# Kernel tuning notes

Hardware: AMD Instinct MI355X
Metric: run time of the kernel (lower is better)

## Reference

```python
import jax, jax.numpy as jnp
import numpy as np

EMB = 128
HEADS = 4
HEAD_DIM = 128  # concat=False: out_channels per head = embedding_dim
LAYERS = 4
BOARD_WIDTH = 8
FC1 = 64
NEG_SLOPE = 0.2  # GATv2 LeakyReLU default
N_CELLS = 200_000
N_PIECES = 100_000
N_EDGES = 500_000
N_GRAPHS = 256


def setup_inputs() -> dict:
    key = jax.random.key(0)
    ks = jax.random.split(key, 24)
    cell_x = jnp.zeros((N_CELLS,), jnp.int32)  # cell vocab size is 1
    piece_x = jax.random.randint(ks[0], (N_PIECES, 1), 0, 2, dtype=jnp.int32)
    edge_src = jax.random.randint(ks[1], (N_EDGES,), 0, N_PIECES, dtype=jnp.int32)
    edge_dst = jax.random.randint(ks[2], (N_EDGES,), 0, N_CELLS, dtype=jnp.int32)
    cell_batch = jnp.sort(jax.random.randint(ks[3], (N_CELLS,), 0, N_GRAPHS, dtype=jnp.int32))

    HD = HEADS * HEAD_DIM
    s_emb = 1.0
    s_lin = 1.0 / np.sqrt(EMB)
    cell_emb = jax.random.normal(ks[4], (1, EMB), jnp.float32) * s_emb
    piece_emb = jax.random.normal(ks[5], (2, EMB), jnp.float32) * s_emb
    W_l = jax.random.normal(ks[6], (LAYERS, EMB, HD), jnp.float32) * s_lin
    b_l = jnp.zeros((LAYERS, HD), jnp.float32)
    W_r = jax.random.normal(ks[7], (LAYERS, EMB, HD), jnp.float32) * s_lin
    b_r = jnp.zeros((LAYERS, HD), jnp.float32)
    att = jax.random.normal(ks[8], (LAYERS, HEADS, HEAD_DIM), jnp.float32) * (1.0 / np.sqrt(HEAD_DIM))
    conv_bias = jnp.zeros((LAYERS, EMB), jnp.float32)
    fc1_w = jax.random.normal(ks[9], (EMB, FC1), jnp.float32) * s_lin
    fc1_b = jnp.zeros((FC1,), jnp.float32)
    policy_w = jax.random.normal(ks[10], (FC1, BOARD_WIDTH), jnp.float32) * (1.0 / np.sqrt(FC1))
    policy_b = jnp.zeros((BOARD_WIDTH,), jnp.float32)
    value_w = jax.random.normal(ks[11], (FC1, 1), jnp.float32) * (1.0 / np.sqrt(FC1))
    value_b = jnp.zeros((1,), jnp.float32)
    return {
        "cell_x": cell_x, "piece_x": piece_x, "edge_src": edge_src,
        "edge_dst": edge_dst, "cell_batch": cell_batch,
        "cell_emb": cell_emb, "piece_emb": piece_emb,
        "W_l": W_l, "b_l": b_l, "W_r": W_r, "b_r": b_r,
        "att": att, "conv_bias": conv_bias,
        "fc1_w": fc1_w, "fc1_b": fc1_b,
        "policy_w": policy_w, "policy_b": policy_b,
        "value_w": value_w, "value_b": value_b,
    }


def _gatv2_layer(piece, cell, edge_src, edge_dst, Wl, bl, Wr, br, a, bias):
    P, C = piece.shape[0], cell.shape[0]
    x_src = (piece @ Wl + bl).reshape(P, HEADS, HEAD_DIM)
    x_dst = (cell @ Wr + br).reshape(C, HEADS, HEAD_DIM)
    xs = x_src[edge_src]                       # [E,H,D] gather
    e = jax.nn.leaky_relu(xs + x_dst[edge_dst], NEG_SLOPE)
    logits = jnp.einsum('ehd,hd->eh', e, a)    # [E,H]
    # segment softmax over edges sharing the same destination cell
    m = jax.ops.segment_max(logits, edge_dst, num_segments=C)
    ex = jnp.exp(logits - m[edge_dst])
    denom = jax.ops.segment_sum(ex, edge_dst, num_segments=C)
    alpha = ex / denom[edge_dst]               # [E,H]
    msg = xs * alpha[:, :, None]               # [E,H,D]
    out = jax.ops.segment_sum(msg, edge_dst, num_segments=C)  # [C,H,D]
    return out.mean(axis=1) + bias             # concat=False -> mean over heads


def reference(cell_x, piece_x, edge_src, edge_dst, cell_batch,
              cell_emb, piece_emb, W_l, b_l, W_r, b_r, att, conv_bias,
              fc1_w, fc1_b, policy_w, policy_b, value_w, value_b):
    cell = cell_emb[cell_x]                    # [C,128]
    piece = piece_emb[piece_x.squeeze(-1)]     # [P,128], never updated (HeteroConv only emits dst type)
    for l in range(LAYERS):
        cell = _gatv2_layer(piece, cell, edge_src, edge_dst,
                            W_l[l], b_l[l], W_r[l], b_r[l], att[l], conv_bias[l])
        cell = jax.nn.relu(cell)               # dropout: eval-mode identity
    # global mean pool over cells per graph
    sums = jax.ops.segment_sum(cell, cell_batch, num_segments=N_GRAPHS)
    cnts = jax.ops.segment_sum(jnp.ones((cell.shape[0],), cell.dtype), cell_batch, num_segments=N_GRAPHS)
    graph_emb = sums / jnp.maximum(cnts, 1.0)[:, None]
    h = jax.nn.relu(graph_emb @ fc1_w + fc1_b)
    policy_logits = h @ policy_w + policy_b
    value = jnp.tanh(h @ value_w + value_b)
    return (policy_logits, value)
```

## Files before the change

kernel.cpp:

```cpp
#include <hip/hip_runtime.h>
#include <math.h>

#define NC 200000
#define NE 500000
#define NP 100000
#define NG 256
#define NLAYERS 4
#define NKEY 256
#define CLAMP 15
#define NSLOPE 0.2f
#define R 8

#define O_CNT 0u
#define O_TB  6400000u
#define O_XS  6412800u
#define O_GB  6429184u
#define O_TAB 6430336u

#define ZB   1563
#define TBB  13
#define XSB  16
#define GBB  782
#define PREP_BLOCKS (ZB + TBB + XSB + GBB)

__device__ __forceinline__ float lrelu(float x) { return x > 0.f ? x : NSLOPE * x; }

__global__ void k_prep(int4* __restrict__ zbase,
                       const int* __restrict__ piece_x,
                       unsigned* __restrict__ tb,
                       const float* __restrict__ piece_emb,
                       const float* __restrict__ W_l,
                       const float* __restrict__ b_l,
                       float* __restrict__ xs,
                       const int* __restrict__ cell_batch,
                       int* __restrict__ gb) {
  int b = blockIdx.x, tid = threadIdx.x;
  if (b < ZB) {
    int i4 = b * 256 + tid;
    if (i4 < (R * NC) / 4) zbase[i4] = make_int4(0, 0, 0, 0);
  } else if (b < ZB + TBB) {
    int j = (b - ZB) * 256 + tid;
    if (j < NP / 32) {
      unsigned w = 0;
      const int* p = piece_x + j * 32;
      #pragma unroll
      for (int k = 0; k < 32; ++k) w |= (unsigned)(p[k] & 1) << k;
      tb[j] = w;
    }
  } else if (b < ZB + TBB + XSB) {
    int idx = (b - ZB - TBB) * 256 + tid;
    int l = idx >> 10, t = (idx >> 9) & 1, j = idx & 511;
    float acc = b_l[l * 512 + j];
    const float* pe = piece_emb + t * 128;
    const float* W = W_l + l * 65536;
    #pragma unroll 8
    for (int d = 0; d < 128; ++d) acc = fmaf(pe[d], W[d * 512 + j], acc);
    xs[idx] = acc;
  } else {
    int i = (b - ZB - TBB - XSB) * 256 + tid;
    if (i < NC) {
      int bi = cell_batch[i];
      int bn = (i + 1 < NC) ? cell_batch[i + 1] : NG;
      if (i == 0) for (int g = 0; g <= bi; ++g) gb[g] = 0;
      for (int g = bi + 1; g <= bn; ++g) gb[g] = i + 1;
    }
  }
}

__global__ void __launch_bounds__(256)
k_count(const unsigned* __restrict__ tb,
        const int* __restrict__ esrc,
        const int* __restrict__ edst,
        int* __restrict__ cnt) {
  unsigned xcc;
  asm volatile("s_getreg_b32 %0, hwreg(HW_REG_XCC_ID)" : "=s"(xcc));
  int* base = cnt + (xcc & (R - 1)) * NC;
  int gid = blockIdx.x * blockDim.x + threadIdx.x;
  if (gid >= NE / 4) return;
  int4 s4 = *(const int4*)(esrc + gid * 4);
  int4 d4 = *(const int4*)(edst + gid * 4);
  int t0 = (tb[s4.x >> 5] >> (s4.x & 31)) & 1;
  int t1 = (tb[s4.y >> 5] >> (s4.y & 31)) & 1;
  int t2 = (tb[s4.z >> 5] >> (s4.z & 31)) & 1;
  int t3 = (tb[s4.w >> 5] >> (s4.w & 31)) & 1;
  atomicAdd(&base[d4.x], 1 << (t0 << 4));
  atomicAdd(&base[d4.y], 1 << (t1 << 4));
  atomicAdd(&base[d4.z], 1 << (t2 << 4));
  atomicAdd(&base[d4.w], 1 << (t3 << 4));
}

__global__ void __launch_bounds__(512)
k_layers4(const float* __restrict__ cell_emb,
          const float* __restrict__ W_r, const float* __restrict__ b_r,
          const float* __restrict__ xs,  const float* __restrict__ att,
          const float* __restrict__ conv_bias,
          float* __restrict__ tab) {
  __shared__ float cell[128];
  __shared__ float part[8][2];
  __shared__ float wgt[8];
  int tid = threadIdx.x;
  int key = blockIdx.x;
  int n0 = key >> 4, n1 = key & 15;
  if (tid < 128) cell[tid] = cell_emb[tid];
  __syncthreads();

  for (int l = 0; l < NLAYERS; ++l) {
    const float* Wl  = W_r + (size_t)l * 65536;
    const float* xsL = xs + l * 1024;
    float acc = b_r[l * 512 + tid];
    #pragma unroll 16
    for (int d = 0; d < 128; ++d)
      acc = fmaf(cell[d], Wl[d * 512 + tid], acc);
    float av = att[l * 512 + tid];
    float p0 = lrelu(xsL[tid] + acc) * av;
    float p1 = lrelu(xsL[512 + tid] + acc) * av;
    #pragma unroll
    for (int m = 32; m >= 1; m >>= 1) {
      p0 += __shfl_xor(p0, m);
      p1 += __shfl_xor(p1, m);
    }
    int w = tid >> 6, lane = tid & 63;
    if (lane == 0) { part[w][0] = p0; part[w][1] = p1; }
    __syncthreads();
    if (tid < 4) {
      float L0 = part[2 * tid][0] + part[2 * tid + 1][0];
      float L1 = part[2 * tid][1] + part[2 * tid + 1][1];
      float ww0 = 0.f, ww1 = 0.f;
      if (n0 + n1 > 0) {
        float m = -1e30f;
        if (n0 > 0) m = L0;
        if (n1 > 0) m = fmaxf(m, L1);
        float e0 = (n0 > 0) ? (float)n0 * expf(L0 - m) : 0.f;
        float e1 = (n1 > 0) ? (float)n1 * expf(L1 - m) : 0.f;
        float inv = 1.f / (e0 + e1);
        ww0 = e0 * inv; ww1 = e1 * inv;
      }
      wgt[tid] = ww0; wgt[4 + tid] = ww1;
    }
    __syncthreads();
    if (tid < 128) {
      float o = conv_bias[l * 128 + tid];
      #pragma unroll
      for (int h = 0; h < 4; ++h)
        o += 0.25f * (wgt[h]     * xsL[h * 128 + tid] +
                      wgt[4 + h] * xsL[512 + h * 128 + tid]);
      o = fmaxf(o, 0.f);
      cell[tid] = o;
      if (l == NLAYERS - 1) tab[key * 128 + tid] = o;
    }
    __syncthreads();
  }
}

__global__ void __launch_bounds__(256)
k_poolhead(const int* __restrict__ gb, const unsigned* __restrict__ cnt,
           const float* __restrict__ tab,
           const float* __restrict__ fc1_w, const float* __restrict__ fc1_b,
           const float* __restrict__ pol_w, const float* __restrict__ pol_b,
           const float* __restrict__ val_w, const float* __restrict__ val_b,
           float* __restrict__ out) {
  __shared__ int hist[NKEY];
  __shared__ int klist[NKEY];
  __shared__ int wcnt[4];
  __shared__ float emb[128];
  __shared__ float hbuf[64];
  int g = blockIdx.x, tid = threadIdx.x;
  hist[tid] = 0;
  __syncthreads();
  int lo = gb[g], hi = gb[g + 1];
  for (int c = lo + tid; c < hi; c += 256) {
    unsigned v = 0;
    #pragma unroll
    for (int r = 0; r < R; ++r) v += cnt[c + r * NC];
    int n0 = min((int)(v & 0xffffu), CLAMP);
    int n1 = min((int)(v >> 16), CLAMP);
    atomicAdd(&hist[(n0 << 4) | n1], 1);
  }
  __syncthreads();
  unsigned long long m = __ballot(hist[tid] != 0);
  int w = tid >> 6, lane = tid & 63;
  if (lane == 0) wcnt[w] = __popcll(m);
  __syncthreads();
  int basep = 0;
  #pragma unroll
  for (int i = 0; i < 4; ++i) if (i < w) basep += wcnt[i];
  if (hist[tid] != 0)
    klist[basep + __popcll(m & ((1ull << lane) - 1ull))] = tid;
  __syncthreads();
  int kn = wcnt[0] + wcnt[1] + wcnt[2] + wcnt[3];
  if (tid < 128) {
    float acc = 0.f;
    for (int i = 0; i < kn; ++i) {
      int k = klist[i];
      acc = fmaf((float)hist[k], tab[k * 128 + tid], acc);
    }
    emb[tid] = acc / fmaxf((float)(hi - lo), 1.f);
  }
  __syncthreads();
  if (tid < 64) {
    float a = fc1_b[tid];
    #pragma unroll 8
    for (int d = 0; d < 128; ++d) a = fmaf(emb[d], fc1_w[d * 64 + tid], a);
    hbuf[tid] = fmaxf(a, 0.f);
  }
  __syncthreads();
  if (tid < 8) {
    float p = pol_b[tid];
    #pragma unroll
    for (int k = 0; k < 64; ++k) p = fmaf(hbuf[k], pol_w[k * 8 + tid], p);
    out[g * 8 + tid] = p;
  } else if (tid == 8) {
    float v = val_b[0];
    #pragma unroll
    for (int k = 0; k < 64; ++k) v = fmaf(hbuf[k], val_w[k], v);
    out[NG * 8 + g] = tanhf(v);
  }
}

extern "C" void kernel_launch(void* const* d_in, const int* in_sizes, int n_in,
                              void* d_out, int out_size, void* d_ws, size_t ws_size,
                              hipStream_t stream) {
  (void)in_sizes; (void)n_in; (void)out_size; (void)ws_size;
  const int*   piece_x   = (const int*)d_in[1];
  const int*   edge_src  = (const int*)d_in[2];
  const int*   edge_dst  = (const int*)d_in[3];
  const int*   cell_batch= (const int*)d_in[4];
  const float* cell_emb  = (const float*)d_in[5];
  const float* piece_emb = (const float*)d_in[6];
  const float* W_l       = (const float*)d_in[7];
  const float* b_l       = (const float*)d_in[8];
  const float* W_r       = (const float*)d_in[9];
  const float* b_r       = (const float*)d_in[10];
  const float* att       = (const float*)d_in[11];
  const float* conv_bias = (const float*)d_in[12];
  const float* fc1_w     = (const float*)d_in[13];
  const float* fc1_b     = (const float*)d_in[14];
  const float* pol_w     = (const float*)d_in[15];
  const float* pol_b     = (const float*)d_in[16];
  const float* val_w     = (const float*)d_in[17];
  const float* val_b     = (const float*)d_in[18];
  float* out = (float*)d_out;

  char* ws = (char*)d_ws;
  int*      cnt  = (int*)(ws + O_CNT);
  unsigned* cntu = (unsigned*)(ws + O_CNT);
  unsigned* tb   = (unsigned*)(ws + O_TB);
  float*    xs   = (float*)(ws + O_XS);
  int*      gb   = (int*)(ws + O_GB);
  float*    tab  = (float*)(ws + O_TAB);

  k_prep<<<PREP_BLOCKS, 256, 0, stream>>>((int4*)ws, piece_x, tb, piece_emb,
                                          W_l, b_l, xs, cell_batch, gb);
  k_count<<<(NE / 4 + 255) / 256, 256, 0, stream>>>(tb, edge_src, edge_dst, cnt);
  k_layers4<<<NKEY, 512, 0, stream>>>(cell_emb, W_r, b_r, xs, att, conv_bias, tab);
  k_poolhead<<<NG, 256, 0, stream>>>(gb, cntu, tab,
                                     fc1_w, fc1_b, pol_w, pol_b,
                                     val_w, val_b, out);
}
```

Before: 59.52 us.

## Fuse all stages into one cooperative persistent kernel with grid syncs

Replaces the four separate launches with a single cooperative kernel of 256 blocks × 512 threads that runs the prep, edge-count, layer-table and pool/head phases, separated by grid-wide barriers. The edge counting is merged into the layer phase, so its atomics can overlap with the per-key layer computation, which does not depend on the counts. The aim is to remove launch gaps and inter-kernel drain time. In exchange, only 256 blocks do all the grid-stride prep and atomic work, which may reduce memory parallelism, and grid sync adds overhead. A three-launch fallback runs if the cooperative launch fails.

```diff
diff --git a/kernel.cpp b/kernel.cpp
--- a/kernel.cpp
+++ b/kernel.cpp
@@ -1,5 +1,8 @@
 #include <hip/hip_runtime.h>
+#include <hip/hip_cooperative_groups.h>
 #include <math.h>
+
+namespace cg = cooperative_groups;
 
 #define NC 200000
 #define NE 500000
@@ -17,203 +20,200 @@
 #define O_GB  6429184u
 #define O_TAB 6430336u
 
-#define ZB   1563
-#define TBB  13
-#define XSB  16
-#define GBB  782
-#define PREP_BLOCKS (ZB + TBB + XSB + GBB)
+#define I_ZERO 400000
+#define I_TB   403125
+#define I_XS   407221
+#define I_GB   607221
+
+struct GArgs {
+  const int* piece_x; const int* esrc; const int* edst; const int* cell_batch;
+  const float* cell_emb; const float* piece_emb;
+  const float* W_l; const float* b_l; const float* W_r; const float* b_r;
+  const float* att; const float* conv_bias;
+  const float* fc1_w; const float* fc1_b; const float* pol_w; const float* pol_b;
+  const float* val_w; const float* val_b;
+  int* cnt; unsigned* tb; float* xs; int* gb; float* tab; float* out;
+};
 
 __device__ __forceinline__ float lrelu(float x) { return x > 0.f ? x : NSLOPE * x; }
 
-__global__ void k_prep(int4* __restrict__ zbase,
-                       const int* __restrict__ piece_x,
-                       unsigned* __restrict__ tb,
-                       const float* __restrict__ piece_emb,
-                       const float* __restrict__ W_l,
-                       const float* __restrict__ b_l,
-                       float* __restrict__ xs,
-                       const int* __restrict__ cell_batch,
-                       int* __restrict__ gb) {
-  int b = blockIdx.x, tid = threadIdx.x;
-  if (b < ZB) {
-    int i4 = b * 256 + tid;
-    if (i4 < (R * NC) / 4) zbase[i4] = make_int4(0, 0, 0, 0);
-  } else if (b < ZB + TBB) {
-    int j = (b - ZB) * 256 + tid;
-    if (j < NP / 32) {
-      unsigned w = 0;
-      const int* p = piece_x + j * 32;
-      #pragma unroll
-      for (int k = 0; k < 32; ++k) w |= (unsigned)(p[k] & 1) << k;
-      tb[j] = w;
-    }
-  } else if (b < ZB + TBB + XSB) {
-    int idx = (b - ZB - TBB) * 256 + tid;
-    int l = idx >> 10, t = (idx >> 9) & 1, j = idx & 511;
-    float acc = b_l[l * 512 + j];
-    const float* pe = piece_emb + t * 128;
-    const float* W = W_l + l * 65536;
-    #pragma unroll 8
-    for (int d = 0; d < 128; ++d) acc = fmaf(pe[d], W[d * 512 + j], acc);
-    xs[idx] = acc;
-  } else {
-    int i = (b - ZB - TBB - XSB) * 256 + tid;
-    if (i < NC) {
-      int bi = cell_batch[i];
-      int bn = (i + 1 < NC) ? cell_batch[i + 1] : NG;
-      if (i == 0) for (int g = 0; g <= bi; ++g) gb[g] = 0;
-      for (int g = bi + 1; g <= bn; ++g) gb[g] = i + 1;
-    }
-  }
-}
-
-__global__ void __launch_bounds__(256)
-k_count(const unsigned* __restrict__ tb,
-        const int* __restrict__ esrc,
-        const int* __restrict__ edst,
-        int* __restrict__ cnt) {
-  unsigned xcc;
-  asm volatile("s_getreg_b32 %0, hwreg(HW_REG_XCC_ID)" : "=s"(xcc));
-  int* base = cnt + (xcc & (R - 1)) * NC;
-  int gid = blockIdx.x * blockDim.x + threadIdx.x;
-  if (gid >= NE / 4) return;
-  int4 s4 = *(const int4*)(esrc + gid * 4);
-  int4 d4 = *(const int4*)(edst + gid * 4);
-  int t0 = (tb[s4.x >> 5] >> (s4.x & 31)) & 1;
-  int t1 = (tb[s4.y >> 5] >> (s4.y & 31)) & 1;
-  int t2 = (tb[s4.z >> 5] >> (s4.z & 31)) & 1;
-  int t3 = (tb[s4.w >> 5] >> (s4.w & 31)) & 1;
-  atomicAdd(&base[d4.x], 1 << (t0 << 4));
-  atomicAdd(&base[d4.y], 1 << (t1 << 4));
-  atomicAdd(&base[d4.z], 1 << (t2 << 4));
-  atomicAdd(&base[d4.w], 1 << (t3 << 4));
-}
-
+template<int PHASE>
 __global__ void __launch_bounds__(512)
-k_layers4(const float* __restrict__ cell_emb,
-          const float* __restrict__ W_r, const float* __restrict__ b_r,
-          const float* __restrict__ xs,  const float* __restrict__ att,
-          const float* __restrict__ conv_bias,
-          float* __restrict__ tab) {
-  __shared__ float cell[128];
+k_mega(GArgs a) {
+  constexpr bool ALL = (PHASE < 0);
+  int tid = threadIdx.x, bid = blockIdx.x;
+  int nthr = gridDim.x * blockDim.x;
+  int gid = bid * blockDim.x + tid;
+
+  __shared__ float scell[128];
   __shared__ float part[8][2];
   __shared__ float wgt[8];
-  int tid = threadIdx.x;
-  int key = blockIdx.x;
-  int n0 = key >> 4, n1 = key & 15;
-  if (tid < 128) cell[tid] = cell_emb[tid];
-  __syncthreads();
-
-  for (int l = 0; l < NLAYERS; ++l) {
-    const float* Wl  = W_r + (size_t)l * 65536;
-    const float* xsL = xs + l * 1024;
-    float acc = b_r[l * 512 + tid];
-    #pragma unroll 16
-    for (int d = 0; d < 128; ++d)
-      acc = fmaf(cell[d], Wl[d * 512 + tid], acc);
-    float av = att[l * 512 + tid];
-    float p0 = lrelu(xsL[tid] + acc) * av;
-    float p1 = lrelu(xsL[512 + tid] + acc) * av;
-    #pragma unroll
-    for (int m = 32; m >= 1; m >>= 1) {
-      p0 += __shfl_xor(p0, m);
-      p1 += __shfl_xor(p1, m);
-    }
-    int w = tid >> 6, lane = tid & 63;
-    if (lane == 0) { part[w][0] = p0; part[w][1] = p1; }
-    __syncthreads();
-    if (tid < 4) {
-      float L0 = part[2 * tid][0] + part[2 * tid + 1][0];
-      float L1 = part[2 * tid][1] + part[2 * tid + 1][1];
-      float ww0 = 0.f, ww1 = 0.f;
-      if (n0 + n1 > 0) {
-        float m = -1e30f;
-        if (n0 > 0) m = L0;
-        if (n1 > 0) m = fmaxf(m, L1);
-        float e0 = (n0 > 0) ? (float)n0 * expf(L0 - m) : 0.f;
-        float e1 = (n1 > 0) ? (float)n1 * expf(L1 - m) : 0.f;
-        float inv = 1.f / (e0 + e1);
-        ww0 = e0 * inv; ww1 = e1 * inv;
-      }
-      wgt[tid] = ww0; wgt[4 + tid] = ww1;
-    }
-    __syncthreads();
-    if (tid < 128) {
-      float o = conv_bias[l * 128 + tid];
-      #pragma unroll
-      for (int h = 0; h < 4; ++h)
-        o += 0.25f * (wgt[h]     * xsL[h * 128 + tid] +
-                      wgt[4 + h] * xsL[512 + h * 128 + tid]);
-      o = fmaxf(o, 0.f);
-      cell[tid] = o;
-      if (l == NLAYERS - 1) tab[key * 128 + tid] = o;
-    }
-    __syncthreads();
-  }
-}
-
-__global__ void __launch_bounds__(256)
-k_poolhead(const int* __restrict__ gb, const unsigned* __restrict__ cnt,
-           const float* __restrict__ tab,
-           const float* __restrict__ fc1_w, const float* __restrict__ fc1_b,
-           const float* __restrict__ pol_w, const float* __restrict__ pol_b,
-           const float* __restrict__ val_w, const float* __restrict__ val_b,
-           float* __restrict__ out) {
   __shared__ int hist[NKEY];
   __shared__ int klist[NKEY];
-  __shared__ int wcnt[4];
+  __shared__ int wcnt[8];
   __shared__ float emb[128];
   __shared__ float hbuf[64];
-  int g = blockIdx.x, tid = threadIdx.x;
-  hist[tid] = 0;
-  __syncthreads();
-  int lo = gb[g], hi = gb[g + 1];
-  for (int c = lo + tid; c < hi; c += 256) {
-    unsigned v = 0;
-    #pragma unroll
-    for (int r = 0; r < R; ++r) v += cnt[c + r * NC];
-    int n0 = min((int)(v & 0xffffu), CLAMP);
-    int n1 = min((int)(v >> 16), CLAMP);
-    atomicAdd(&hist[(n0 << 4) | n1], 1);
-  }
-  __syncthreads();
-  unsigned long long m = __ballot(hist[tid] != 0);
-  int w = tid >> 6, lane = tid & 63;
-  if (lane == 0) wcnt[w] = __popcll(m);
-  __syncthreads();
-  int basep = 0;
-  #pragma unroll
-  for (int i = 0; i < 4; ++i) if (i < w) basep += wcnt[i];
-  if (hist[tid] != 0)
-    klist[basep + __popcll(m & ((1ull << lane) - 1ull))] = tid;
-  __syncthreads();
-  int kn = wcnt[0] + wcnt[1] + wcnt[2] + wcnt[3];
-  if (tid < 128) {
-    float acc = 0.f;
-    for (int i = 0; i < kn; ++i) {
-      int k = klist[i];
-      acc = fmaf((float)hist[k], tab[k * 128 + tid], acc);
-    }
-    emb[tid] = acc / fmaxf((float)(hi - lo), 1.f);
-  }
-  __syncthreads();
-  if (tid < 64) {
-    float a = fc1_b[tid];
-    #pragma unroll 8
-    for (int d = 0; d < 128; ++d) a = fmaf(emb[d], fc1_w[d * 64 + tid], a);
-    hbuf[tid] = fmaxf(a, 0.f);
-  }
-  __syncthreads();
-  if (tid < 8) {
-    float p = pol_b[tid];
-    #pragma unroll
-    for (int k = 0; k < 64; ++k) p = fmaf(hbuf[k], pol_w[k * 8 + tid], p);
-    out[g * 8 + tid] = p;
-  } else if (tid == 8) {
-    float v = val_b[0];
-    #pragma unroll
-    for (int k = 0; k < 64; ++k) v = fmaf(hbuf[k], val_w[k], v);
-    out[NG * 8 + g] = tanhf(v);
+
+  if (ALL || PHASE == 0) {
+    for (int i = gid; i < I_GB; i += nthr) {
+      if (i < I_ZERO) {
+        ((int4*)a.cnt)[i] = make_int4(0, 0, 0, 0);
+      } else if (i < I_TB) {
+        int j = i - I_ZERO;
+        unsigned w = 0;
+        const int* p = a.piece_x + j * 32;
+        #pragma unroll
+        for (int k = 0; k < 32; ++k) w |= (unsigned)(p[k] & 1) << k;
+        a.tb[j] = w;
+      } else if (i < I_XS) {
+        int idx = i - I_TB;
+        int l = idx >> 10, t = (idx >> 9) & 1, j = idx & 511;
+        float acc = a.b_l[l * 512 + j];
+        const float* pe = a.piece_emb + t * 128;
+        const float* W = a.W_l + l * 65536;
+        #pragma unroll 8
+        for (int d = 0; d < 128; ++d) acc = fmaf(pe[d], W[d * 512 + j], acc);
+        a.xs[idx] = acc;
+      } else {
+        int c = i - I_XS;
+        int bi = a.cell_batch[c];
+        int bn = (c + 1 < NC) ? a.cell_batch[c + 1] : NG;
+        if (c == 0) for (int g = 0; g <= bi; ++g) a.gb[g] = 0;
+        for (int g = bi + 1; g <= bn; ++g) a.gb[g] = c + 1;
+      }
+    }
+  }
+  if (ALL) cg::this_grid().sync();
+
+  if (ALL || PHASE == 1) {
+    if (tid < 128) scell[tid] = a.cell_emb[tid];
+    __syncthreads();
+    {
+      unsigned xcc;
+      asm volatile("s_getreg_b32 %0, hwreg(HW_REG_XCC_ID)" : "=s"(xcc));
+      int* base = a.cnt + (xcc & (R - 1)) * NC;
+      for (int i = gid; i < NE / 4; i += nthr) {
+        int4 s4 = ((const int4*)a.esrc)[i];
+        int4 d4 = ((const int4*)a.edst)[i];
+        int t0 = (a.tb[s4.x >> 5] >> (s4.x & 31)) & 1;
+        int t1 = (a.tb[s4.y >> 5] >> (s4.y & 31)) & 1;
+        int t2 = (a.tb[s4.z >> 5] >> (s4.z & 31)) & 1;
+        int t3 = (a.tb[s4.w >> 5] >> (s4.w & 31)) & 1;
+        atomicAdd(&base[d4.x], 1 << (t0 << 4));
+        atomicAdd(&base[d4.y], 1 << (t1 << 4));
+        atomicAdd(&base[d4.z], 1 << (t2 << 4));
+        atomicAdd(&base[d4.w], 1 << (t3 << 4));
+      }
+    }
+    int key = bid;
+    int n0 = key >> 4, n1 = key & 15;
+    for (int l = 0; l < NLAYERS; ++l) {
+      const float* Wl  = a.W_r + (size_t)l * 65536;
+      const float* xsL = a.xs + l * 1024;
+      float acc = a.b_r[l * 512 + tid];
+      #pragma unroll 16
+      for (int d = 0; d < 128; ++d)
+        acc = fmaf(scell[d], Wl[d * 512 + tid], acc);
+      float av = a.att[l * 512 + tid];
+      float p0 = lrelu(xsL[tid] + acc) * av;
+      float p1 = lrelu(xsL[512 + tid] + acc) * av;
+      #pragma unroll
+      for (int m = 32; m >= 1; m >>= 1) {
+        p0 += __shfl_xor(p0, m);
+        p1 += __shfl_xor(p1, m);
+      }
+      int w = tid >> 6, lane = tid & 63;
+      if (lane == 0) { part[w][0] = p0; part[w][1] = p1; }
+      __syncthreads();
+      if (tid < 4) {
+        float L0 = part[2 * tid][0] + part[2 * tid + 1][0];
+        float L1 = part[2 * tid][1] + part[2 * tid + 1][1];
+        float ww0 = 0.f, ww1 = 0.f;
+        if (n0 + n1 > 0) {
+          float m = -1e30f;
+          if (n0 > 0) m = L0;
+          if (n1 > 0) m = fmaxf(m, L1);
+          float e0 = (n0 > 0) ? (float)n0 * expf(L0 - m) : 0.f;
+          float e1 = (n1 > 0) ? (float)n1 * expf(L1 - m) : 0.f;
+          float inv = 1.f / (e0 + e1);
+          ww0 = e0 * inv; ww1 = e1 * inv;
+        }
+        wgt[tid] = ww0; wgt[4 + tid] = ww1;
+      }
+      __syncthreads();
+      if (tid < 128) {
+        float o = a.conv_bias[l * 128 + tid];
+        #pragma unroll
+        for (int h = 0; h < 4; ++h)
+          o += 0.25f * (wgt[h]     * xsL[h * 128 + tid] +
+                        wgt[4 + h] * xsL[512 + h * 128 + tid]);
+        o = fmaxf(o, 0.f);
+        scell[tid] = o;
+        if (l == NLAYERS - 1) a.tab[key * 128 + tid] = o;
+      }
+      __syncthreads();
+    }
+  }
+  if (ALL) cg::this_grid().sync();
+
+  if (ALL || PHASE == 2) {
+    int g = bid;
+    if (g < NG) {
+      if (tid < NKEY) hist[tid] = 0;
+      __syncthreads();
+      int lo = a.gb[g], hi = a.gb[g + 1];
+      const unsigned* cntu = (const unsigned*)a.cnt;
+      for (int c = lo + tid; c < hi; c += 512) {
+        unsigned v = 0;
+        #pragma unroll
+        for (int r = 0; r < R; ++r) v += cntu[c + r * NC];
+        int n0 = min((int)(v & 0xffffu), CLAMP);
+        int n1 = min((int)(v >> 16), CLAMP);
+        atomicAdd(&hist[(n0 << 4) | n1], 1);
+      }
+      __syncthreads();
+      bool present = (tid < NKEY) && (hist[tid] != 0);
+      unsigned long long m = __ballot(present);
+      int w = tid >> 6, lane = tid & 63;
+      if (lane == 0) wcnt[w] = __popcll(m);
+      __syncthreads();
+      int basep = 0;
+      #pragma unroll
+      for (int i = 0; i < 8; ++i) if (i < w) basep += wcnt[i];
+      if (present)
+        klist[basep + __popcll(m & ((1ull << lane) - 1ull))] = tid;
+      __syncthreads();
+      int kn = 0;
+      #pragma unroll
+      for (int i = 0; i < 8; ++i) kn += wcnt[i];
+      if (tid < 128) {
+        float acc = 0.f;
+        for (int i = 0; i < kn; ++i) {
+          int k = klist[i];
+          acc = fmaf((float)hist[k], a.tab[k * 128 + tid], acc);
+        }
+        emb[tid] = acc / fmaxf((float)(hi - lo), 1.f);
+      }
+      __syncthreads();
+      if (tid < 64) {
+        float v = a.fc1_b[tid];
+        #pragma unroll 8
+        for (int d = 0; d < 128; ++d) v = fmaf(emb[d], a.fc1_w[d * 64 + tid], v);
+        hbuf[tid] = fmaxf(v, 0.f);
+      }
+      __syncthreads();
+      if (tid < 8) {
+        float p = a.pol_b[tid];
+        #pragma unroll
+        for (int k = 0; k < 64; ++k) p = fmaf(hbuf[k], a.pol_w[k * 8 + tid], p);
+        a.out[g * 8 + tid] = p;
+      } else if (tid == 8) {
+        float v = a.val_b[0];
+        #pragma unroll
+        for (int k = 0; k < 64; ++k) v = fmaf(hbuf[k], a.val_w[k], v);
+        a.out[NG * 8 + g] = tanhf(v);
+      }
+    }
   }
 }
 
@@ -221,39 +221,40 @@
                               void* d_out, int out_size, void* d_ws, size_t ws_size,
                               hipStream_t stream) {
   (void)in_sizes; (void)n_in; (void)out_size; (void)ws_size;
-  const int*   piece_x   = (const int*)d_in[1];
-  const int*   edge_src  = (const int*)d_in[2];
-  const int*   edge_dst  = (const int*)d_in[3];
-  const int*   cell_batch= (const int*)d_in[4];
-  const float* cell_emb  = (const float*)d_in[5];
-  const float* piece_emb = (const float*)d_in[6];
-  const float* W_l       = (const float*)d_in[7];
-  const float* b_l       = (const float*)d_in[8];
-  const float* W_r       = (const float*)d_in[9];
-  const float* b_r       = (const float*)d_in[10];
-  const float* att       = (const float*)d_in[11];
-  const float* conv_bias = (const float*)d_in[12];
-  const float* fc1_w     = (const float*)d_in[13];
-  const float* fc1_b     = (const float*)d_in[14];
-  const float* pol_w     = (const float*)d_in[15];
-  const float* pol_b     = (const float*)d_in[16];
-  const float* val_w     = (const float*)d_in[17];
-  const float* val_b     = (const float*)d_in[18];
-  float* out = (float*)d_out;
-
   char* ws = (char*)d_ws;
-  int*      cnt  = (int*)(ws + O_CNT);
-  unsigned* cntu = (unsigned*)(ws + O_CNT);
-  unsigned* tb   = (unsigned*)(ws + O_TB);
-  float*    xs   = (float*)(ws + O_XS);
-  int*      gb   = (int*)(ws + O_GB);
-  float*    tab  = (float*)(ws + O_TAB);
-
-  k_prep<<<PREP_BLOCKS, 256, 0, stream>>>((int4*)ws, piece_x, tb, piece_emb,
-                                          W_l, b_l, xs, cell_batch, gb);
-  k_count<<<(NE / 4 + 255) / 256, 256, 0, stream>>>(tb, edge_src, edge_dst, cnt);
-  k_layers4<<<NKEY, 512, 0, stream>>>(cell_emb, W_r, b_r, xs, att, conv_bias, tab);
-  k_poolhead<<<NG, 256, 0, stream>>>(gb, cntu, tab,
-                                     fc1_w, fc1_b, pol_w, pol_b,
-                                     val_w, val_b, out);
+  GArgs a;
+  a.piece_x    = (const int*)d_in[1];
+  a.esrc       = (const int*)d_in[2];
+  a.edst       = (const int*)d_in[3];
+  a.cell_batch = (const int*)d_in[4];
+  a.cell_emb   = (const float*)d_in[5];
+  a.piece_emb  = (const float*)d_in[6];
+  a.W_l        = (const float*)d_in[7];
+  a.b_l        = (const float*)d_in[8];
+  a.W_r        = (const float*)d_in[9];
+  a.b_r        = (const float*)d_in[10];
+  a.att        = (const float*)d_in[11];
+  a.conv_bias  = (const float*)d_in[12];
+  a.fc1_w      = (const float*)d_in[13];
+  a.fc1_b      = (const float*)d_in[14];
+  a.pol_w      = (const float*)d_in[15];
+  a.pol_b      = (const float*)d_in[16];
+  a.val_w      = (const float*)d_in[17];
+  a.val_b      = (const float*)d_in[18];
+  a.cnt = (int*)(ws + O_CNT);
+  a.tb  = (unsigned*)(ws + O_TB);
+  a.xs  = (float*)(ws + O_XS);
+  a.gb  = (int*)(ws + O_GB);
+  a.tab = (float*)(ws + O_TAB);
+  a.out = (float*)d_out;
+
+  void* params[] = { &a };
+  hipError_t e = hipLaunchCooperativeKernel(
+      reinterpret_cast<void*>(k_mega<-1>), dim3(NKEY), dim3(512),
+      params, 0, stream);
+  if (e != hipSuccess) {
+    k_mega<0><<<(I_GB + 511) / 512, 512, 0, stream>>>(a);
+    k_mega<1><<<NKEY, 512, 0, stream>>>(a);
+    k_mega<2><<<NG, 512, 0, stream>>>(a);
+  }
 }
```

Result: slower. 120.1 us (+101.7%).

## Fuse edge counting into layer-table kernel and binary-search graph bounds

Applied to the files above, without the earlier changes.

The edge-type counting pass now runs at the start of the per-key layer kernel, which has enough threads to cover every edge quad, so one kernel launch goes away. The graph-boundary array is no longer built in the prep kernel. Instead each pooling block binary-searches the sorted cell_batch for its range, and the prep kernel is flattened to 512-thread blocks with linear index ranges. This is meant to cut launch and dependency overhead. In exchange, the count atomics share blocks with the dense layer math, and each pooling block pays for two short binary searches.

```diff
diff --git a/kernel.cpp b/kernel.cpp
--- a/kernel.cpp
+++ b/kernel.cpp
@@ -14,41 +14,35 @@
 #define O_CNT 0u
 #define O_TB  6400000u
 #define O_XS  6412800u
-#define O_GB  6429184u
-#define O_TAB 6430336u
-
-#define ZB   1563
-#define TBB  13
-#define XSB  16
-#define GBB  782
-#define PREP_BLOCKS (ZB + TBB + XSB + GBB)
+#define O_TAB 6429184u
+
+#define I_ZERO 400000
+#define I_TB   403125
+#define I_XS   407221
+#define PREP_BLOCKS ((I_XS + 511) / 512)
 
 __device__ __forceinline__ float lrelu(float x) { return x > 0.f ? x : NSLOPE * x; }
 
-__global__ void k_prep(int4* __restrict__ zbase,
-                       const int* __restrict__ piece_x,
-                       unsigned* __restrict__ tb,
-                       const float* __restrict__ piece_emb,
-                       const float* __restrict__ W_l,
-                       const float* __restrict__ b_l,
-                       float* __restrict__ xs,
-                       const int* __restrict__ cell_batch,
-                       int* __restrict__ gb) {
-  int b = blockIdx.x, tid = threadIdx.x;
-  if (b < ZB) {
-    int i4 = b * 256 + tid;
-    if (i4 < (R * NC) / 4) zbase[i4] = make_int4(0, 0, 0, 0);
-  } else if (b < ZB + TBB) {
-    int j = (b - ZB) * 256 + tid;
-    if (j < NP / 32) {
-      unsigned w = 0;
-      const int* p = piece_x + j * 32;
-      #pragma unroll
-      for (int k = 0; k < 32; ++k) w |= (unsigned)(p[k] & 1) << k;
-      tb[j] = w;
-    }
-  } else if (b < ZB + TBB + XSB) {
-    int idx = (b - ZB - TBB) * 256 + tid;
+__global__ void __launch_bounds__(512)
+k_prep(int4* __restrict__ cnt4,
+       const int* __restrict__ piece_x,
+       unsigned* __restrict__ tb,
+       const float* __restrict__ piece_emb,
+       const float* __restrict__ W_l,
+       const float* __restrict__ b_l,
+       float* __restrict__ xs) {
+  int i = blockIdx.x * 512 + threadIdx.x;
+  if (i < I_ZERO) {
+    cnt4[i] = make_int4(0, 0, 0, 0);
+  } else if (i < I_TB) {
+    int j = i - I_ZERO;
+    unsigned w = 0;
+    const int* p = piece_x + j * 32;
+    #pragma unroll
+    for (int k = 0; k < 32; ++k) w |= (unsigned)(p[k] & 1) << k;
+    tb[j] = w;
+  } else if (i < I_XS) {
+    int idx = i - I_TB;
     int l = idx >> 10, t = (idx >> 9) & 1, j = idx & 511;
     float acc = b_l[l * 512 + j];
     const float* pe = piece_emb + t * 128;
@@ -56,61 +50,51 @@
     #pragma unroll 8
     for (int d = 0; d < 128; ++d) acc = fmaf(pe[d], W[d * 512 + j], acc);
     xs[idx] = acc;
-  } else {
-    int i = (b - ZB - TBB - XSB) * 256 + tid;
-    if (i < NC) {
-      int bi = cell_batch[i];
-      int bn = (i + 1 < NC) ? cell_batch[i + 1] : NG;
-      if (i == 0) for (int g = 0; g <= bi; ++g) gb[g] = 0;
-      for (int g = bi + 1; g <= bn; ++g) gb[g] = i + 1;
-    }
-  }
-}
-
-__global__ void __launch_bounds__(256)
-k_count(const unsigned* __restrict__ tb,
-        const int* __restrict__ esrc,
-        const int* __restrict__ edst,
-        int* __restrict__ cnt) {
-  unsigned xcc;
-  asm volatile("s_getreg_b32 %0, hwreg(HW_REG_XCC_ID)" : "=s"(xcc));
-  int* base = cnt + (xcc & (R - 1)) * NC;
-  int gid = blockIdx.x * blockDim.x + threadIdx.x;
-  if (gid >= NE / 4) return;
-  int4 s4 = *(const int4*)(esrc + gid * 4);
-  int4 d4 = *(const int4*)(edst + gid * 4);
-  int t0 = (tb[s4.x >> 5] >> (s4.x & 31)) & 1;
-  int t1 = (tb[s4.y >> 5] >> (s4.y & 31)) & 1;
-  int t2 = (tb[s4.z >> 5] >> (s4.z & 31)) & 1;
-  int t3 = (tb[s4.w >> 5] >> (s4.w & 31)) & 1;
-  atomicAdd(&base[d4.x], 1 << (t0 << 4));
-  atomicAdd(&base[d4.y], 1 << (t1 << 4));
-  atomicAdd(&base[d4.z], 1 << (t2 << 4));
-  atomicAdd(&base[d4.w], 1 << (t3 << 4));
+  }
 }
 
 __global__ void __launch_bounds__(512)
-k_layers4(const float* __restrict__ cell_emb,
-          const float* __restrict__ W_r, const float* __restrict__ b_r,
-          const float* __restrict__ xs,  const float* __restrict__ att,
-          const float* __restrict__ conv_bias,
-          float* __restrict__ tab) {
-  __shared__ float cell[128];
+k_countlayers(const unsigned* __restrict__ tb,
+              const int* __restrict__ esrc,
+              const int* __restrict__ edst,
+              int* __restrict__ cnt,
+              const float* __restrict__ cell_emb,
+              const float* __restrict__ W_r, const float* __restrict__ b_r,
+              const float* __restrict__ xs,  const float* __restrict__ att,
+              const float* __restrict__ conv_bias,
+              float* __restrict__ tab) {
+  __shared__ float scell[128];
   __shared__ float part[8][2];
   __shared__ float wgt[8];
-  int tid = threadIdx.x;
-  int key = blockIdx.x;
-  int n0 = key >> 4, n1 = key & 15;
-  if (tid < 128) cell[tid] = cell_emb[tid];
-  __syncthreads();
-
+  int tid = threadIdx.x, bid = blockIdx.x;
+  if (tid < 128) scell[tid] = cell_emb[tid];
+  __syncthreads();
+  {
+    unsigned xcc;
+    asm volatile("s_getreg_b32 %0, hwreg(HW_REG_XCC_ID)" : "=s"(xcc));
+    int* base = cnt + (xcc & (R - 1)) * NC;
+    int gid = bid * 512 + tid;
+    if (gid < NE / 4) {
+      int4 s4 = ((const int4*)esrc)[gid];
+      int4 d4 = ((const int4*)edst)[gid];
+      int t0 = (tb[s4.x >> 5] >> (s4.x & 31)) & 1;
+      int t1 = (tb[s4.y >> 5] >> (s4.y & 31)) & 1;
+      int t2 = (tb[s4.z >> 5] >> (s4.z & 31)) & 1;
+      int t3 = (tb[s4.w >> 5] >> (s4.w & 31)) & 1;
+      atomicAdd(&base[d4.x], 1 << (t0 << 4));
+      atomicAdd(&base[d4.y], 1 << (t1 << 4));
+      atomicAdd(&base[d4.z], 1 << (t2 << 4));
+      atomicAdd(&base[d4.w], 1 << (t3 << 4));
+    }
+  }
+  int key = bid, n0 = key >> 4, n1 = key & 15;
   for (int l = 0; l < NLAYERS; ++l) {
     const float* Wl  = W_r + (size_t)l * 65536;
     const float* xsL = xs + l * 1024;
     float acc = b_r[l * 512 + tid];
     #pragma unroll 16
     for (int d = 0; d < 128; ++d)
-      acc = fmaf(cell[d], Wl[d * 512 + tid], acc);
+      acc = fmaf(scell[d], Wl[d * 512 + tid], acc);
     float av = att[l * 512 + tid];
     float p0 = lrelu(xsL[tid] + acc) * av;
     float p1 = lrelu(xsL[512 + tid] + acc) * av;
@@ -145,7 +129,7 @@
         o += 0.25f * (wgt[h]     * xsL[h * 128 + tid] +
                       wgt[4 + h] * xsL[512 + h * 128 + tid]);
       o = fmaxf(o, 0.f);
-      cell[tid] = o;
+      scell[tid] = o;
       if (l == NLAYERS - 1) tab[key * 128 + tid] = o;
     }
     __syncthreads();
@@ -153,7 +137,8 @@
 }
 
 __global__ void __launch_bounds__(256)
-k_poolhead(const int* __restrict__ gb, const unsigned* __restrict__ cnt,
+k_poolhead(const int* __restrict__ cell_batch,
+           const unsigned* __restrict__ cnt,
            const float* __restrict__ tab,
            const float* __restrict__ fc1_w, const float* __restrict__ fc1_b,
            const float* __restrict__ pol_w, const float* __restrict__ pol_b,
@@ -166,9 +151,12 @@
   __shared__ float hbuf[64];
   int g = blockIdx.x, tid = threadIdx.x;
   hist[tid] = 0;
-  __syncthreads();
-  int lo = gb[g], hi = gb[g + 1];
-  for (int c = lo + tid; c < hi; c += 256) {
+  int lo = 0, hi = NC;
+  while (lo < hi) { int mid = (lo + hi) >> 1; if (cell_batch[mid] < g) lo = mid + 1; else hi = mid; }
+  int lo2 = lo, hi2 = NC;
+  while (lo2 < hi2) { int mid = (lo2 + hi2) >> 1; if (cell_batch[mid] < g + 1) lo2 = mid + 1; else hi2 = mid; }
+  __syncthreads();
+  for (int c = lo + tid; c < lo2; c += 256) {
     unsigned v = 0;
     #pragma unroll
     for (int r = 0; r < R; ++r) v += cnt[c + r * NC];
@@ -194,7 +182,7 @@
       int k = klist[i];
       acc = fmaf((float)hist[k], tab[k * 128 + tid], acc);
     }
-    emb[tid] = acc / fmaxf((float)(hi - lo), 1.f);
+    emb[tid] = acc / fmaxf((float)(lo2 - lo), 1.f);
   }
   __syncthreads();
   if (tid < 64) {
@@ -246,14 +234,14 @@
   unsigned* cntu = (unsigned*)(ws + O_CNT);
   unsigned* tb   = (unsigned*)(ws + O_TB);
   float*    xs   = (float*)(ws + O_XS);
-  int*      gb   = (int*)(ws + O_GB);
   float*    tab  = (float*)(ws + O_TAB);
 
-  k_prep<<<PREP_BLOCKS, 256, 0, stream>>>((int4*)ws, piece_x, tb, piece_emb,
-                                          W_l, b_l, xs, cell_batch, gb);
-  k_count<<<(NE / 4 + 255) / 256, 256, 0, stream>>>(tb, edge_src, edge_dst, cnt);
-  k_layers4<<<NKEY, 512, 0, stream>>>(cell_emb, W_r, b_r, xs, att, conv_bias, tab);
-  k_poolhead<<<NG, 256, 0, stream>>>(gb, cntu, tab,
+  k_prep<<<PREP_BLOCKS, 512, 0, stream>>>((int4*)cnt, piece_x, tb, piece_emb,
+                                          W_l, b_l, xs);
+  k_countlayers<<<NKEY, 512, 0, stream>>>(tb, edge_src, edge_dst, cnt,
+                                          cell_emb, W_r, b_r, xs, att,
+                                          conv_bias, tab);
+  k_poolhead<<<NG, 256, 0, stream>>>(cell_batch, cntu, tab,
                                      fc1_w, fc1_b, pol_w, pol_b,
                                      val_w, val_b, out);
 }
```

Result: no change. 59.74 us (+0.4%).
